# Kernel tuning notes

Hardware: AMD Instinct MI355X
Metric: run time of the kernel (lower is better)

## Reference

```python
import jax, jax.numpy as jnp
import numpy as np
from jax import lax

H = 300  # L1 = L2 = 300 in the source


def setup_inputs() -> dict:
    key = jax.random.key(0)
    ks = jax.random.split(key, 10)
    B = 1024
    oplen = 256
    s = 1.0 / np.sqrt(H)
    return {
        "h0": jax.random.normal(ks[0], (B, H), jnp.float32),
        "c0": jax.random.normal(ks[1], (B, H), jnp.float32),
        "start": jax.random.normal(ks[2], (B, H), jnp.float32),
        # LSTMCell params (PyTorch layout: [4H, H] weights, [4H] biases; gate order i,f,g,o)
        "W_ih": jax.random.normal(ks[3], (4 * H, H), jnp.float32) * s,
        "W_hh": jax.random.normal(ks[4], (4 * H, H), jnp.float32) * s,
        "b_ih": jax.random.normal(ks[5], (4 * H,), jnp.float32) * s,
        "b_hh": jax.random.normal(ks[6], (4 * H,), jnp.float32) * s,
        # output Linear [H, H]
        "W_out": jax.random.normal(ks[7], (H, H), jnp.float32) * s,
        "b_out": jax.random.normal(ks[8], (H,), jnp.float32) * s,
        "oplen": oplen,
    }


def reference(h0, c0, start, W_ih, W_hh, b_ih, b_hh, W_out, b_out, oplen):
    def step(carry, _):
        h, c, x = carry
        # LSTMCell: gates = x W_ih^T + b_ih + h W_hh^T + b_hh
        gates = x @ W_ih.T + b_ih + h @ W_hh.T + b_hh  # [B, 4H]
        i, f, g, o = jnp.split(gates, 4, axis=-1)
        i = jax.nn.sigmoid(i)
        f = jax.nn.sigmoid(f)
        g = jnp.tanh(g)
        o = jax.nn.sigmoid(o)
        c_new = f * c + i * g
        h_new = o * jnp.tanh(c_new)
        out = h_new @ W_out.T + b_out  # fed back as next input
        return (h_new, c_new, out), out

    _, outs = lax.scan(step, (h0, c0, start), None, length=oplen)
    return outs  # [oplen, B, H]
```

## Files before the change

### kernel.cpp

```cpp
#include <hip/hip_runtime.h>
#include <hip/hip_bf16.h>


typedef __attribute__((ext_vector_type(8))) short bf16x8;
typedef __attribute__((ext_vector_type(4))) float f32x4;
typedef __attribute__((ext_vector_type(2))) unsigned long long u64x2;
typedef unsigned long long u64;

#define MFMA16(a, b, c) __builtin_amdgcn_mfma_f32_16x16x32_bf16((a), (b), (c), 0, 0, 0)

__device__ __forceinline__ float sigf(float x) { return 1.0f / (1.0f + __expf(-x)); }
__device__ __forceinline__ float tanh_fast(float x) { return 2.0f / (1.0f + __expf(-2.0f * x)) - 1.0f; }
__device__ __forceinline__ short f2bf(float x) { __hip_bfloat16 h = __float2bfloat16(x); return *(short*)&h; }
__device__ __forceinline__ float bf2f(short s) { __hip_bfloat16 h; *(short*)&h = s; return __bfloat162float(h); }

__device__ __forceinline__ u64 lda8(const u64* p) {
    return __hip_atomic_load(p, __ATOMIC_RELAXED, __HIP_MEMORY_SCOPE_AGENT);
}
__device__ __forceinline__ void sta8(u64* p, u64 v) {
    __hip_atomic_store(p, v, __ATOMIC_RELAXED, __HIP_MEMORY_SCOPE_AGENT);
}

__global__ void build_kernel(const float* __restrict__ W_out, const float* __restrict__ b_out,
                             float* __restrict__ W_big, float* __restrict__ bias_big,
                             unsigned int* __restrict__ hfrag_zero, unsigned int* __restrict__ flags) {
    int stride = gridDim.x * blockDim.x;
    int idx = blockIdx.x * blockDim.x + threadIdx.x;
    for (int i = idx; i < 655360; i += stride) hfrag_zero[i] = 0u;
    for (int i = idx; i < 300 * 300; i += stride) W_big[1200 * 300 + i] = W_out[i];
    for (int i = idx; i < 300; i += stride) bias_big[1200 + i] = b_out[i];
    if (idx < 256) flags[idx] = 0u;
}

__global__ __launch_bounds__(128) void fold_kernel(const float* __restrict__ W_ih,
                                                   const float* __restrict__ W_hh,
                                                   const float* __restrict__ W_out,
                                                   float* __restrict__ W_big) {
    int j = blockIdx.x;
    __shared__ float row[300];
    for (int m = threadIdx.x; m < 300; m += 128) row[m] = W_ih[j * 300 + m];
    __syncthreads();
    int k0 = threadIdx.x, k1 = threadIdx.x + 128, k2 = threadIdx.x + 256;
    float a0 = 0.f, a1 = 0.f, a2 = 0.f;
    for (int m = 0; m < 300; ++m) {
        float w = row[m];
        a0 += w * W_out[m * 300 + k0];
        a1 += w * W_out[m * 300 + k1];
        if (k2 < 300) a2 += w * W_out[m * 300 + k2];
    }
    W_big[j * 300 + k0] = W_hh[j * 300 + k0] + a0;
    W_big[j * 300 + k1] = W_hh[j * 300 + k1] + a1;
    if (k2 < 300) W_big[j * 300 + k2] = W_hh[j * 300 + k2] + a2;
}

__global__ __launch_bounds__(64) void bias_fold_kernel(const float* __restrict__ W_ih,
                                                       const float* __restrict__ b_ih,
                                                       const float* __restrict__ b_hh,
                                                       const float* __restrict__ b_out,
                                                       float* __restrict__ bias_big) {
    int j = blockIdx.x;
    int lane = threadIdx.x;
    float s = 0.f;
    for (int m = lane; m < 300; m += 64) s += W_ih[j * 300 + m] * b_out[m];
    for (int off = 32; off > 0; off >>= 1) s += __shfl_down(s, off);
    if (lane == 0) bias_big[j] = b_ih[j] + b_hh[j] + s;
}

__global__ __launch_bounds__(64) void pack_w_kernel(const float* __restrict__ W_big,
                                                    short* __restrict__ Wh, short* __restrict__ Wl) {
    int tile = blockIdx.x;
    int jt = tile / 50;
    int rem = tile - jt * 50;
    int ch = rem / 10;
    int kc = rem - ch * 10;
    int lane = threadIdx.x;
    int j = jt * 16 + (lane & 15);
    int kbase = kc * 32 + (lane >> 4) * 8;
    int r = (ch < 4) ? (ch * 300 + j) : (1200 + j);
    size_t base = (size_t)tile * 512 + (size_t)lane * 8;
#pragma unroll
    for (int jj = 0; jj < 8; ++jj) {
        int k = kbase + jj;
        float v = (j < 300 && k < 300) ? W_big[(size_t)r * 300 + k] : 0.f;
        short hi = f2bf(v);
        short lo = f2bf(v - bf2f(hi));
        Wh[base + jj] = hi;
        Wl[base + jj] = lo;
    }
}

__global__ __launch_bounds__(128) void step0_kernel(
    const float* __restrict__ x_in, const float* __restrict__ h_in,
    const float* __restrict__ W_ih, const float* __restrict__ W_hh,
    const float* __restrict__ b_ih, const float* __restrict__ b_hh,
    const float* __restrict__ c_in, float* __restrict__ c_out,
    float* __restrict__ h_out) {
    __shared__ float hs[16][68];
    __shared__ float wsm[16][32];
    const int t = threadIdx.x;
    const int bm0 = blockIdx.x * 64;
    const int jg0 = blockIdx.y * 8;

    const int row_idx = t & 31;
    const int wkq = (t >> 5) << 2;
    const int jl = row_idx >> 2, g = row_idx & 3;
    const int grow = jg0 + jl + 300 * g;
    const bool wvalid = (jg0 + jl) < 300;

    float acc[4][4];
#pragma unroll
    for (int i = 0; i < 4; ++i)
#pragma unroll
        for (int q = 0; q < 4; ++q) acc[i][q] = 0.f;

    for (int it = 0; it < 38; ++it) {
        const int k0 = it << 4;
#pragma unroll
        for (int q = 0; q < 2; ++q) {
            int qi = t + q * 128;
            int bl = qi >> 2;
            int kq = (qi & 3) << 2;
            int kg = k0 + kq;
            float4 hv = make_float4(0.f, 0.f, 0.f, 0.f);
            if (kg < 600) {
                const float* src = (kg < 300) ? (x_in + (size_t)(bm0 + bl) * 300 + kg)
                                              : (h_in + (size_t)(bm0 + bl) * 300 + (kg - 300));
                hv = *(const float4*)src;
            }
            hs[kq + 0][bl] = hv.x;
            hs[kq + 1][bl] = hv.y;
            hs[kq + 2][bl] = hv.z;
            hs[kq + 3][bl] = hv.w;
        }
        {
            int kg = k0 + wkq;
            float4 wv = make_float4(0.f, 0.f, 0.f, 0.f);
            if (wvalid && kg < 600) {
                const float* src = (kg < 300) ? (W_ih + (size_t)grow * 300 + kg)
                                              : (W_hh + (size_t)grow * 300 + (kg - 300));
                wv = *(const float4*)src;
            }
            wsm[wkq + 0][row_idx] = wv.x;
            wsm[wkq + 1][row_idx] = wv.y;
            wsm[wkq + 2][row_idx] = wv.z;
            wsm[wkq + 3][row_idx] = wv.w;
        }
        __syncthreads();
        const int bs4 = (t & 15) << 2;
        const int c4 = (t >> 4) << 2;
#pragma unroll
        for (int k = 0; k < 16; ++k) {
            float4 hv = *(const float4*)&hs[k][bs4];
            float4 wv = *(const float4*)&wsm[k][c4];
            float hvv[4] = {hv.x, hv.y, hv.z, hv.w};
            float wvv[4] = {wv.x, wv.y, wv.z, wv.w};
#pragma unroll
            for (int bi = 0; bi < 4; ++bi)
#pragma unroll
                for (int q = 0; q < 4; ++q) acc[bi][q] += hvv[bi] * wvv[q];
        }
        __syncthreads();
    }

    const int b0 = bm0 + ((t & 15) << 2);
    const int j = jg0 + (t >> 4);
    if (j < 300) {
        const float bi_ = b_ih[j] + b_hh[j];
        const float bf_ = b_ih[j + 300] + b_hh[j + 300];
        const float bg_ = b_ih[j + 600] + b_hh[j + 600];
        const float bo_ = b_ih[j + 900] + b_hh[j + 900];
#pragma unroll
        for (int bi = 0; bi < 4; ++bi) {
            const int b = b0 + bi;
            float ig = sigf(acc[bi][0] + bi_);
            float fg = sigf(acc[bi][1] + bf_);
            float gg = tanh_fast(acc[bi][2] + bg_);
            float og = sigf(acc[bi][3] + bo_);
            float cn = fg * c_in[(size_t)b * 300 + j] + ig * gg;
            c_out[(size_t)b * 300 + j] = cn;
            h_out[(size_t)b * 300 + j] = og * tanh_fast(cn);
        }
    }
}

__global__ __launch_bounds__(256) void convert_h_kernel(const float* __restrict__ h_row,
                                                        short* __restrict__ Hh, short* __restrict__ Hl) {
    int idx = blockIdx.x * 256 + threadIdx.x;
    int m = idx / 320;
    int k = idx - m * 320;
    float v = (k < 300) ? h_row[(size_t)m * 300 + k] : 0.f;
    short hi = f2bf(v);
    short lo = f2bf(v - bf2f(hi));
    int chunk = k >> 5;
    int lane = (m & 15) + 16 * ((k & 31) >> 3);
    int slot = k & 7;
    size_t fi = (((size_t)(m >> 4) * 10 + chunk) * 64 + lane) * 8 + slot;
    Hh[fi] = hi;
    Hl[fi] = lo;
}

__global__ __launch_bounds__(256, 1) void persist_kernel(
    short* __restrict__ H0h, short* __restrict__ H0l,
    short* __restrict__ H1h, short* __restrict__ H1l,
    const short* __restrict__ Wph, const short* __restrict__ Wpl,
    const float* __restrict__ bias, const float* __restrict__ c_init,
    float* __restrict__ out, unsigned* __restrict__ flags) {
    __shared__ __align__(16) short w_hi[50 * 512];
    __shared__ __align__(16) short w_lo[40 * 512];
    __shared__ __align__(16) short hst_h[2048];
    __shared__ __align__(16) short hst_l[2048];

    const int bid = blockIdx.x;
    const int g = bid / 19;
    const int jt = bid - g * 19;
    const int tid = threadIdx.x;
    const int wave = tid >> 6;
    const int lane = tid & 63;

    {
        const int4* s1 = (const int4*)(Wph + (size_t)jt * 25600);
        int4* d1 = (int4*)w_hi;
        for (int i = tid; i < 3200; i += 256) d1[i] = s1[i];
        const int4* s2 = (const int4*)(Wpl + (size_t)jt * 25600);
        int4* d2 = (int4*)w_lo;
        for (int i = tid; i < 2560; i += 256) d2[i] = s2[i];
    }

    const int jl = lane & 15;
    const int jg = jt * 16 + jl;
    const bool jvalid = jg < 300;
    const int mr = (lane >> 4) << 2;
    const int laneo = lane << 3;

    float b_i = 0.f, b_f = 0.f, b_g = 0.f, b_o = 0.f, b_y = 0.f;
    if (jvalid) {
        b_i = bias[jg];
        b_f = bias[300 + jg];
        b_g = bias[600 + jg];
        b_o = bias[900 + jg];
        b_y = bias[1200 + jg];
    }

    const int mt0 = g * 8 + wave;
    float c_reg[8];
#pragma unroll
    for (int mti = 0; mti < 2; ++mti)
#pragma unroll
        for (int r = 0; r < 4; ++r) {
            const int m = (mt0 + 4 * mti) * 16 + mr + r;
            c_reg[mti * 4 + r] = jvalid ? c_init[(size_t)m * 300 + jg] : 0.f;
        }

    const int iA2 = (mt0 * 640 + lane) * 2;
    const int chunk = jt >> 1;
    unsigned* fpoll_p = flags + (g * 19 + (lane < 19 ? lane : 18));
    unsigned* fpub_p = flags + (g * 19 + jt);

    const int so_mtl = tid >> 5;
    const int so_mrow = (tid >> 1) & 15;
    const int so_ha = tid & 1;
    const int so_off = ((so_mtl * 16 + so_mrow) * 2 + so_ha) * 8;
    const size_t so_bi =
        ((size_t)((g * 8 + so_mtl) * 10 + chunk) * 64 + (so_mrow + ((2 * (jt & 1) + so_ha) << 4))) * 2;

    __syncthreads();

#pragma unroll 1
    for (int tt = 1; tt <= 256; ++tt) {
        const short* Ah8 = (tt & 1) ? H0h : H1h;
        const short* Al8 = (tt & 1) ? H0l : H1l;
        short* Bh8 = (tt & 1) ? H1h : H0h;
        short* Bl8 = (tt & 1) ? H1l : H0l;
        float* yo = out + (size_t)(tt - 1) * 307200;

        if (wave == 0) {
            const unsigned target = (unsigned)(tt - 1);
            while (true) {
                unsigned fv = __hip_atomic_load(fpoll_p, __ATOMIC_RELAXED,
                                                __HIP_MEMORY_SCOPE_AGENT);
                if (__all((int)((lane >= 19) | (fv >= target)))) break;
                __builtin_amdgcn_s_sleep(1);
            }
        }
        __syncthreads();

        const u64* A2h = (const u64*)Ah8 + iA2;
        const u64* A2l = (const u64*)Al8 + iA2;

        f32x4 acc[4][2];
        f32x4 accy[2];
#pragma unroll
        for (int ch = 0; ch < 4; ++ch) {
            acc[ch][0] = (f32x4){0.f, 0.f, 0.f, 0.f};
            acc[ch][1] = (f32x4){0.f, 0.f, 0.f, 0.f};
        }
        accy[0] = (f32x4){0.f, 0.f, 0.f, 0.f};
        accy[1] = (f32x4){0.f, 0.f, 0.f, 0.f};

        u64x2 p0h[3], p0l[3], p1h[3], p1l[3];
#pragma unroll
        for (int k = 0; k < 2; ++k) {
            p0h[k].x = lda8(A2h + k * 128);
            p0h[k].y = lda8(A2h + k * 128 + 1);
            p0l[k].x = lda8(A2l + k * 128);
            p0l[k].y = lda8(A2l + k * 128 + 1);
            p1h[k].x = lda8(A2h + 5120 + k * 128);
            p1h[k].y = lda8(A2h + 5120 + k * 128 + 1);
            p1l[k].x = lda8(A2l + 5120 + k * 128);
            p1l[k].y = lda8(A2l + 5120 + k * 128 + 1);
        }

#pragma unroll
        for (int kc = 0; kc < 10; ++kc) {
            const int cs = kc % 3;
            if (kc + 2 < 10) {
                const int ns = (kc + 2) % 3;
                p0h[ns].x = lda8(A2h + (kc + 2) * 128);
                p0h[ns].y = lda8(A2h + (kc + 2) * 128 + 1);
                p0l[ns].x = lda8(A2l + (kc + 2) * 128);
                p0l[ns].y = lda8(A2l + (kc + 2) * 128 + 1);
                p1h[ns].x = lda8(A2h + 5120 + (kc + 2) * 128);
                p1h[ns].y = lda8(A2h + 5120 + (kc + 2) * 128 + 1);
                p1l[ns].x = lda8(A2l + 5120 + (kc + 2) * 128);
                p1l[ns].y = lda8(A2l + 5120 + (kc + 2) * 128 + 1);
            }
            const bf16x8 a0h = (bf16x8)p0h[cs];
            const bf16x8 a0l = (bf16x8)p0l[cs];
            const bf16x8 a1h = (bf16x8)p1h[cs];
            const bf16x8 a1l = (bf16x8)p1l[cs];
#pragma unroll
            for (int ch = 0; ch < 4; ++ch) {
                const bf16x8 bh = *(const bf16x8*)(w_hi + ((ch * 10 + kc) << 9) + laneo);
                const bf16x8 bl = *(const bf16x8*)(w_lo + ((ch * 10 + kc) << 9) + laneo);
                acc[ch][0] = MFMA16(a0h, bh, acc[ch][0]);
                acc[ch][0] = MFMA16(a0l, bh, acc[ch][0]);
                acc[ch][0] = MFMA16(a0h, bl, acc[ch][0]);
                acc[ch][1] = MFMA16(a1h, bh, acc[ch][1]);
                acc[ch][1] = MFMA16(a1l, bh, acc[ch][1]);
                acc[ch][1] = MFMA16(a1h, bl, acc[ch][1]);
            }
            const bf16x8 by = *(const bf16x8*)(w_hi + ((40 + kc) << 9) + laneo);
            accy[0] = MFMA16(a0h, by, accy[0]);
            accy[0] = MFMA16(a0l, by, accy[0]);
            accy[1] = MFMA16(a1h, by, accy[1]);
            accy[1] = MFMA16(a1l, by, accy[1]);
        }

#pragma unroll
        for (int mti = 0; mti < 2; ++mti) {
            const int mt_l = wave + 4 * mti;
            const int MT = mt0 + 4 * mti;
#pragma unroll
            for (int r = 0; r < 4; ++r) {
                const float gi = acc[0][mti][r] + b_i;
                const float gf = acc[1][mti][r] + b_f;
                const float gg = acc[2][mti][r] + b_g;
                const float go_ = acc[3][mti][r] + b_o;
                const float iv = sigf(gi), fv = sigf(gf), gv = tanh_fast(gg), ov = sigf(go_);
                const float cn = fv * c_reg[mti * 4 + r] + iv * gv;
                c_reg[mti * 4 + r] = cn;
                const float hv = ov * tanh_fast(cn);
                if (jvalid) {
                    const int m = MT * 16 + mr + r;
                    __builtin_nontemporal_store(accy[mti][r] + b_y, yo + (size_t)m * 300 + jg);
                }
                const short hb = f2bf(hv);
                const short lb = f2bf(hv - bf2f(hb));
                const int si = ((mt_l * 16 + (mr + r)) * 2 + (jl >> 3)) * 8 + (jl & 7);
                hst_h[si] = hb;
                hst_l[si] = lb;
            }
        }
        __syncthreads();

        {
            const u64* sh = (const u64*)&hst_h[so_off];
            const u64* sl = (const u64*)&hst_l[so_off];
            sta8((u64*)Bh8 + so_bi, sh[0]);
            sta8((u64*)Bh8 + so_bi + 1, sh[1]);
            sta8((u64*)Bl8 + so_bi, sl[0]);
            sta8((u64*)Bl8 + so_bi + 1, sl[1]);
        }
        asm volatile("s_waitcnt vmcnt(0)" ::: "memory");
        __syncthreads();
        if (tid == 0) {
            __hip_atomic_store(fpub_p, (unsigned)tt, __ATOMIC_RELAXED,
                               __HIP_MEMORY_SCOPE_AGENT);
        }
    }
}

extern "C" void kernel_launch(void* const* d_in, const int* in_sizes, int n_in,
                              void* d_out, int out_size, void* d_ws, size_t ws_size,
                              hipStream_t stream) {
    const float* h0 = (const float*)d_in[0];
    const float* c0 = (const float*)d_in[1];
    const float* start = (const float*)d_in[2];
    const float* W_ih = (const float*)d_in[3];
    const float* W_hh = (const float*)d_in[4];
    const float* b_ih = (const float*)d_in[5];
    const float* b_hh = (const float*)d_in[6];
    const float* W_out = (const float*)d_in[7];
    const float* b_out = (const float*)d_in[8];
    float* out = (float*)d_out;

    float* wsf = (float*)d_ws;
    float* W_big = wsf;
    float* bias_big = wsf + 450000;
    float* c_ws = wsf + 451504;
    float* h_row = wsf + 758704;
    short* wss = (short*)(wsf + 1065904);
    short* Wh = wss;
    short* Wl = wss + 486400;
    short* H0h = wss + 972800;
    short* H0l = wss + 1300480;
    short* H1h = wss + 1628160;
    short* H1l = wss + 1955840;
    unsigned* flags = (unsigned*)(wss + 2283520);

    build_kernel<<<2816, 256, 0, stream>>>(W_out, b_out, W_big, bias_big, (unsigned int*)H0h, flags);
    fold_kernel<<<1200, 128, 0, stream>>>(W_ih, W_hh, W_out, W_big);
    bias_fold_kernel<<<1200, 64, 0, stream>>>(W_ih, b_ih, b_hh, b_out, bias_big);
    pack_w_kernel<<<950, 64, 0, stream>>>(W_big, Wh, Wl);

    step0_kernel<<<dim3(16, 38), 128, 0, stream>>>(start, h0, W_ih, W_hh, b_ih, b_hh,
                                                   c0, c_ws, h_row);
    convert_h_kernel<<<1280, 256, 0, stream>>>(h_row, H0h, H0l);

    persist_kernel<<<152, 256, 0, stream>>>(H0h, H0l, H1h, H1l, Wh, Wl,
                                            bias_big, c_ws, out, flags);
}
```

Measured before the change: 2.611 ms.

## Replace block-level sync with per-wave flags and defer output stores

Each wave now polls and publishes its own per-wave flag (4x more flags) instead of wave 0 polling and the whole block synchronizing, removing three __syncthreads per step. The h-fragment staging in shared memory is split per wave so only a wave barrier is needed before the global store. All ten A-fragment loads are issued up front instead of a 3-deep rolling prefetch, and the y output stores are moved after the flag publish to shorten the critical path. This raises register pressure and adds more flag polling traffic.

Measured after the change: 3.145 ms. 1.2x slower.

```diff
diff --git a/kernel.cpp b/kernel.cpp
--- a/kernel.cpp
+++ b/kernel.cpp
@@ -29,7 +29,7 @@
     for (int i = idx; i < 655360; i += stride) hfrag_zero[i] = 0u;
     for (int i = idx; i < 300 * 300; i += stride) W_big[1200 * 300 + i] = W_out[i];
     for (int i = idx; i < 300; i += stride) bias_big[1200 + i] = b_out[i];
-    if (idx < 256) flags[idx] = 0u;
+    if (idx < 1024) flags[idx] = 0u;
 }
 
 __global__ __launch_bounds__(128) void fold_kernel(const float* __restrict__ W_ih,
@@ -207,8 +207,8 @@
     float* __restrict__ out, unsigned* __restrict__ flags) {
     __shared__ __align__(16) short w_hi[50 * 512];
     __shared__ __align__(16) short w_lo[40 * 512];
-    __shared__ __align__(16) short hst_h[2048];
-    __shared__ __align__(16) short hst_l[2048];
+    __shared__ __align__(16) short hst_h[4][512];
+    __shared__ __align__(16) short hst_l[4][512];
 
     const int bid = blockIdx.x;
     const int g = bid / 19;
@@ -253,15 +253,16 @@
 
     const int iA2 = (mt0 * 640 + lane) * 2;
     const int chunk = jt >> 1;
-    unsigned* fpoll_p = flags + (g * 19 + (lane < 19 ? lane : 18));
-    unsigned* fpub_p = flags + (g * 19 + jt);
-
-    const int so_mtl = tid >> 5;
-    const int so_mrow = (tid >> 1) & 15;
-    const int so_ha = tid & 1;
-    const int so_off = ((so_mtl * 16 + so_mrow) * 2 + so_ha) * 8;
+    unsigned* fpoll_p = flags + ((g * 19 + (lane < 19 ? lane : 18)) * 4 + wave);
+    unsigned* fpub_p = flags + ((g * 19 + jt) * 4 + wave);
+
+    const int so_tile = lane >> 5;
+    const int so_row = (lane >> 1) & 15;
+    const int so_half = lane & 1;
+    const int so_off = (so_tile * 16 + so_row) * 16 + so_half * 8;
     const size_t so_bi =
-        ((size_t)((g * 8 + so_mtl) * 10 + chunk) * 64 + (so_mrow + ((2 * (jt & 1) + so_ha) << 4))) * 2;
+        ((size_t)((mt0 + 4 * so_tile) * 10 + chunk) * 64 +
+         (so_row + ((2 * (jt & 1) + so_half) << 4))) * 2;
 
     __syncthreads();
 
@@ -273,7 +274,7 @@
         short* Bl8 = (tt & 1) ? H1l : H0l;
         float* yo = out + (size_t)(tt - 1) * 307200;
 
-        if (wave == 0) {
+        {
             const unsigned target = (unsigned)(tt - 1);
             while (true) {
                 unsigned fv = __hip_atomic_load(fpoll_p, __ATOMIC_RELAXED,
@@ -282,10 +283,22 @@
                 __builtin_amdgcn_s_sleep(1);
             }
         }
-        __syncthreads();
 
         const u64* A2h = (const u64*)Ah8 + iA2;
         const u64* A2l = (const u64*)Al8 + iA2;
+
+        u64 f0h[10][2], f0l[10][2], f1h[10][2], f1l[10][2];
+#pragma unroll
+        for (int kc = 0; kc < 10; ++kc) {
+            f0h[kc][0] = lda8(A2h + kc * 128);
+            f0h[kc][1] = lda8(A2h + kc * 128 + 1);
+            f0l[kc][0] = lda8(A2l + kc * 128);
+            f0l[kc][1] = lda8(A2l + kc * 128 + 1);
+            f1h[kc][0] = lda8(A2h + 5120 + kc * 128);
+            f1h[kc][1] = lda8(A2h + 5120 + kc * 128 + 1);
+            f1l[kc][0] = lda8(A2l + 5120 + kc * 128);
+            f1l[kc][1] = lda8(A2l + 5120 + kc * 128 + 1);
+        }
 
         f32x4 acc[4][2];
         f32x4 accy[2];
@@ -297,37 +310,17 @@
         accy[0] = (f32x4){0.f, 0.f, 0.f, 0.f};
         accy[1] = (f32x4){0.f, 0.f, 0.f, 0.f};
 
-        u64x2 p0h[3], p0l[3], p1h[3], p1l[3];
-#pragma unroll
-        for (int k = 0; k < 2; ++k) {
-            p0h[k].x = lda8(A2h + k * 128);
-            p0h[k].y = lda8(A2h + k * 128 + 1);
-            p0l[k].x = lda8(A2l + k * 128);
-            p0l[k].y = lda8(A2l + k * 128 + 1);
-            p1h[k].x = lda8(A2h + 5120 + k * 128);
-            p1h[k].y = lda8(A2h + 5120 + k * 128 + 1);
-            p1l[k].x = lda8(A2l + 5120 + k * 128);
-            p1l[k].y = lda8(A2l + 5120 + k * 128 + 1);
-        }
-
 #pragma unroll
         for (int kc = 0; kc < 10; ++kc) {
-            const int cs = kc % 3;
-            if (kc + 2 < 10) {
-                const int ns = (kc + 2) % 3;
-                p0h[ns].x = lda8(A2h + (kc + 2) * 128);
-                p0h[ns].y = lda8(A2h + (kc + 2) * 128 + 1);
-                p0l[ns].x = lda8(A2l + (kc + 2) * 128);
-                p0l[ns].y = lda8(A2l + (kc + 2) * 128 + 1);
-                p1h[ns].x = lda8(A2h + 5120 + (kc + 2) * 128);
-                p1h[ns].y = lda8(A2h + 5120 + (kc + 2) * 128 + 1);
-                p1l[ns].x = lda8(A2l + 5120 + (kc + 2) * 128);
-                p1l[ns].y = lda8(A2l + 5120 + (kc + 2) * 128 + 1);
-            }
-            const bf16x8 a0h = (bf16x8)p0h[cs];
-            const bf16x8 a0l = (bf16x8)p0l[cs];
-            const bf16x8 a1h = (bf16x8)p1h[cs];
-            const bf16x8 a1l = (bf16x8)p1l[cs];
+            u64x2 t0h, t0l, t1h, t1l;
+            t0h.x = f0h[kc][0]; t0h.y = f0h[kc][1];
+            t0l.x = f0l[kc][0]; t0l.y = f0l[kc][1];
+            t1h.x = f1h[kc][0]; t1h.y = f1h[kc][1];
+            t1l.x = f1l[kc][0]; t1l.y = f1l[kc][1];
+            const bf16x8 a0h = (bf16x8)t0h;
+            const bf16x8 a0l = (bf16x8)t0l;
+            const bf16x8 a1h = (bf16x8)t1h;
+            const bf16x8 a1l = (bf16x8)t1l;
 #pragma unroll
             for (int ch = 0; ch < 4; ++ch) {
                 const bf16x8 bh = *(const bf16x8*)(w_hi + ((ch * 10 + kc) << 9) + laneo);
@@ -348,8 +341,6 @@
 
 #pragma unroll
         for (int mti = 0; mti < 2; ++mti) {
-            const int mt_l = wave + 4 * mti;
-            const int MT = mt0 + 4 * mti;
 #pragma unroll
             for (int r = 0; r < 4; ++r) {
                 const float gi = acc[0][mti][r] + b_i;
@@ -360,32 +351,39 @@
                 const float cn = fv * c_reg[mti * 4 + r] + iv * gv;
                 c_reg[mti * 4 + r] = cn;
                 const float hv = ov * tanh_fast(cn);
-                if (jvalid) {
-                    const int m = MT * 16 + mr + r;
-                    __builtin_nontemporal_store(accy[mti][r] + b_y, yo + (size_t)m * 300 + jg);
-                }
                 const short hb = f2bf(hv);
                 const short lb = f2bf(hv - bf2f(hb));
-                const int si = ((mt_l * 16 + (mr + r)) * 2 + (jl >> 3)) * 8 + (jl & 7);
-                hst_h[si] = hb;
-                hst_l[si] = lb;
+                const int si = (mti * 16 + mr + r) * 16 + jl;
+                hst_h[wave][si] = hb;
+                hst_l[wave][si] = lb;
             }
         }
-        __syncthreads();
+        __builtin_amdgcn_wave_barrier();
+        asm volatile("s_waitcnt lgkmcnt(0)" ::: "memory");
+        __builtin_amdgcn_sched_barrier(0);
 
         {
-            const u64* sh = (const u64*)&hst_h[so_off];
-            const u64* sl = (const u64*)&hst_l[so_off];
+            const u64* sh = (const u64*)&hst_h[wave][so_off];
+            const u64* sl = (const u64*)&hst_l[wave][so_off];
             sta8((u64*)Bh8 + so_bi, sh[0]);
             sta8((u64*)Bh8 + so_bi + 1, sh[1]);
             sta8((u64*)Bl8 + so_bi, sl[0]);
             sta8((u64*)Bl8 + so_bi + 1, sl[1]);
         }
         asm volatile("s_waitcnt vmcnt(0)" ::: "memory");
-        __syncthreads();
-        if (tid == 0) {
+        if (lane == 0) {
             __hip_atomic_store(fpub_p, (unsigned)tt, __ATOMIC_RELAXED,
                                __HIP_MEMORY_SCOPE_AGENT);
+        }
+
+        if (jvalid) {
+#pragma unroll
+            for (int mti = 0; mti < 2; ++mti)
+#pragma unroll
+                for (int r = 0; r < 4; ++r) {
+                    const int m = (mt0 + 4 * mti) * 16 + mr + r;
+                    __builtin_nontemporal_store(accy[mti][r] + b_y, yo + (size_t)m * 300 + jg);
+                }
         }
     }
 }
```
